# Optimization experiments

Measured on AMD Instinct MI355X. Metric: run time of the kernel, lower is better.

## Reference

```python
import jax, jax.numpy as jnp
import numpy as np

N = 120000   # hits
K = 512      # non-noise objects (ids 1..K; id 0 = noise)
D = 8        # cluster-space dim
C = 6        # pid classes
Q_MIN = 1.0
NOISE_THR = 0
PAYLOAD_W = 1.0
EPS = 1e-9


def setup_inputs() -> dict:
    key = jax.random.key(0)
    ks = jax.random.split(key, 9)
    beta = jax.random.uniform(ks[0], (N,), dtype=jnp.float32) * 0.95 + 0.01  # keep arctanh finite
    x = jax.random.normal(ks[1], (N, D), dtype=jnp.float32)
    object_id = jax.random.randint(ks[2], (N,), 0, K + 1).astype(jnp.int32)
    # guarantee every object id (and noise id 0) appears at least once
    object_id = object_id.at[: K + 1].set(jnp.arange(K + 1, dtype=jnp.int32))
    energy = jax.random.normal(ks[3], (N,), dtype=jnp.float32)
    energy_per_hit = jax.random.normal(ks[4], (N,), dtype=jnp.float32)
    momentum = jax.random.normal(ks[5], (N, 3), dtype=jnp.float32)
    momentum_per_hit = jax.random.normal(ks[6], (N, 3), dtype=jnp.float32)
    pid_logits = jax.random.normal(ks[7], (N, C), dtype=jnp.float32)
    pid_per_hit = jax.random.randint(ks[8], (N,), 0, C).astype(jnp.int32)
    return dict(beta=beta, x=x, object_id=object_id, energy=energy,
                energy_per_hit=energy_per_hit, momentum=momentum,
                momentum_per_hit=momentum_per_hit, pid_logits=pid_logits,
                pid_per_hit=pid_per_hit)


def _oc_core(beta, x, object_id):
    """condensation_loss_tiger with weights=1, max_n_rep=0 (no repulsive sampling)."""
    oids = jnp.arange(1, K + 1, dtype=object_id.dtype)
    att_mask = object_id[:, None] == oids[None, :]              # [N, K]
    q = jnp.arctanh(beta) ** 2 + Q_MIN                          # [N]
    alphas = jnp.argmax(q[:, None] * att_mask, axis=0)          # [K] condensation points
    x_k = x[alphas]                                             # [K, D]
    q_k = q[alphas]                                             # [K]
    # squared euclidean distance via gemm (avoids [N,K,D] intermediate)
    d2 = (jnp.sum(x * x, axis=1)[:, None] + jnp.sum(x_k * x_k, axis=1)[None, :]
          - 2.0 * (x @ x_k.T))
    d2 = jnp.maximum(d2, 0.0)                                   # [N, K]
    dist = jnp.sqrt(jnp.maximum(d2, 1e-12))
    qw = q[:, None] * q_k[None, :]                              # [N, K]
    # attractive: per-object normalized by hits in object, then mean over objects
    att_norm = jnp.sum(att_mask, axis=0).astype(x.dtype)        # [K]
    v_att = jnp.sum(jnp.where(att_mask, qw * d2, 0.0) / (att_norm + EPS)[None, :]) / K
    # repulsive: hinge (1 - dist), normalized by n_hits not in object
    rep_mask = (~att_mask) & (dist < 1.0)
    n_rep_k = jnp.sum(~att_mask, axis=0).astype(x.dtype)        # [K]
    n_rep = jnp.sum(rep_mask)
    v_rep = jnp.sum(jnp.where(rep_mask, qw * (1.0 - dist), 0.0) / (n_rep_k + EPS)[None, :]) / K
    l_coward = jnp.mean(1.0 - beta[alphas])
    noise_m = (object_id <= NOISE_THR).astype(beta.dtype)
    l_noise = jnp.sum(beta * noise_m) / jnp.sum(noise_m)
    return v_att, v_rep, l_coward, l_noise, n_rep


def reference(beta, x, object_id, energy, energy_per_hit, momentum,
              momentum_per_hit, pid_logits, pid_per_hit):
    v_att, v_rep, l_coward, l_noise, n_rep = _oc_core(beta, x, object_id)
    oc_total = v_att + v_rep + l_coward + l_noise
    # payload losses on non-noise hits (masked means == F.*_loss on gathered rows)
    m = (object_id > NOISE_THR).astype(beta.dtype)              # [N]
    nm = jnp.sum(m)
    e_loss = jnp.sum((energy - energy_per_hit) ** 2 * m) / nm
    p_loss = jnp.sum((momentum - momentum_per_hit) ** 2 * m[:, None]) / (nm * momentum.shape[1])
    logp = jax.nn.log_softmax(pid_logits, axis=-1)              # [N, C]
    nll = -jnp.take_along_axis(logp, pid_per_hit[:, None], axis=1)[:, 0]
    pid_loss = jnp.sum(nll * m) / nm
    total = oc_total + PAYLOAD_W * (e_loss + p_loss + pid_loss)
    return (v_att, v_rep, l_coward, l_noise, n_rep.astype(jnp.float32),
            oc_total, e_loss, p_loss, pid_loss, total)
```

## Files before the change

kernel.cpp:

```cpp
#include <hip/hip_runtime.h>
#include <math.h>

#define KOBJ 512
#define KTW 8
#define TK 32
#define NTILE (KOBJ / TK)
#define HB 8
#define HCH (256 * HB)
#define MPREP 128

typedef _Float16 half2_t __attribute__((ext_vector_type(2)));

#define AGS(p, v) __hip_atomic_store((p), (v), __ATOMIC_RELAXED, __HIP_MEMORY_SCOPE_AGENT)
#define AGL(p)    __hip_atomic_load((p), __ATOMIC_RELAXED, __HIP_MEMORY_SCOPE_AGENT)

__device__ __forceinline__ float wave_red_f(float v) {
  #pragma unroll
  for (int off = 32; off > 0; off >>= 1) v += __shfl_down(v, off, 64);
  return v;
}

__device__ __forceinline__ float q_of_beta(float b) {
  float a = 0.5f * __logf((1.f + b) / (1.f - b));
  return fmaf(a, a, 1.f);
}

__device__ __forceinline__ float dot8h(uint4 kx, const uint* y, float acc) {
#if __has_builtin(__builtin_amdgcn_fdot2)
  acc = __builtin_amdgcn_fdot2(__builtin_bit_cast(half2_t, y[0]),
                               __builtin_bit_cast(half2_t, kx.x), acc, false);
  acc = __builtin_amdgcn_fdot2(__builtin_bit_cast(half2_t, y[1]),
                               __builtin_bit_cast(half2_t, kx.y), acc, false);
  acc = __builtin_amdgcn_fdot2(__builtin_bit_cast(half2_t, y[2]),
                               __builtin_bit_cast(half2_t, kx.z), acc, false);
  acc = __builtin_amdgcn_fdot2(__builtin_bit_cast(half2_t, y[3]),
                               __builtin_bit_cast(half2_t, kx.w), acc, false);
#else
  const uint kk[4] = {kx.x, kx.y, kx.z, kx.w};
  #pragma unroll
  for (int c = 0; c < 4; c++) {
    half2_t a = __builtin_bit_cast(half2_t, y[c]);
    half2_t b = __builtin_bit_cast(half2_t, kk[c]);
    acc = fmaf((float)a.x, (float)b.x, acc);
    acc = fmaf((float)a.y, (float)b.y, acc);
  }
#endif
  return acc;
}

__global__ __launch_bounds__(256) void
k_prep(const float* __restrict__ beta, const int* __restrict__ oid,
       const float* __restrict__ energy, const float* __restrict__ eph,
       const float* __restrict__ mom, const float* __restrict__ mph,
       const float* __restrict__ logits, const int* __restrict__ pid,
       unsigned long long* __restrict__ amax_part,
       unsigned* __restrict__ cnt_part,
       float* __restrict__ scal_part,
       unsigned* __restrict__ done_cnt, int n) {
  __shared__ unsigned long long lmax[KOBJ];
  __shared__ unsigned lcnt[KOBJ];
  if (blockIdx.x == 0 && threadIdx.x == 0) *done_cnt = 0u;
  for (int t = threadIdx.x; t < KOBJ; t += 256) { lmax[t] = 0ull; lcnt[t] = 0u; }
  __syncthreads();

  float e_t = 0.f, p_t = 0.f, pid_t = 0.f, noise_t = 0.f, ncnt = 0.f, mcnt = 0.f;
  for (int i = blockIdx.x * 256 + threadIdx.x; i < n; i += MPREP * 256) {
    float b = beta[i];
    int o = oid[i];
    if (o > 0) {
      float q = q_of_beta(b);
      unsigned long long key = ((unsigned long long)__float_as_uint(q) << 32)
                             | (unsigned long long)(unsigned)(~(unsigned)i);
      atomicMax(&lmax[o - 1], key);
      atomicAdd(&lcnt[o - 1], 1u);
      mcnt += 1.f;
      float de = energy[i] - eph[i];
      e_t = fmaf(de, de, e_t);
      float p0 = mom[3*i+0] - mph[3*i+0];
      float p1 = mom[3*i+1] - mph[3*i+1];
      float p2 = mom[3*i+2] - mph[3*i+2];
      p_t = fmaf(p0, p0, p_t); p_t = fmaf(p1, p1, p_t); p_t = fmaf(p2, p2, p_t);
      const float* lg = logits + 6*i;
      float l0=lg[0], l1=lg[1], l2=lg[2], l3=lg[3], l4=lg[4], l5=lg[5];
      float mx = fmaxf(fmaxf(fmaxf(l0,l1),fmaxf(l2,l3)), fmaxf(l4,l5));
      float s = __expf(l0-mx)+__expf(l1-mx)+__expf(l2-mx)
              + __expf(l3-mx)+__expf(l4-mx)+__expf(l5-mx);
      int pc = pid[i];
      float lp = (pc==0)?l0:(pc==1)?l1:(pc==2)?l2:(pc==3)?l3:(pc==4)?l4:l5;
      pid_t += mx + __logf(s) - lp;
    } else {
      noise_t += b;
      ncnt += 1.f;
    }
  }
  __syncthreads();

  for (int t = threadIdx.x; t < KOBJ; t += 256) {
    amax_part[(size_t)blockIdx.x * KOBJ + t] = lmax[t];
    cnt_part[(size_t)blockIdx.x * KOBJ + t]  = lcnt[t];
  }

  float vals[6] = {e_t, p_t, pid_t, noise_t, ncnt, mcnt};
  #pragma unroll
  for (int j = 0; j < 6; j++) vals[j] = wave_red_f(vals[j]);
  __shared__ float sred[4][6];
  int w = threadIdx.x >> 6, l = threadIdx.x & 63;
  if (l == 0) {
    #pragma unroll
    for (int j = 0; j < 6; j++) sred[w][j] = vals[j];
  }
  __syncthreads();
  if (threadIdx.x == 0) {
    #pragma unroll
    for (int j = 0; j < 6; j++)
      scal_part[blockIdx.x * 8 + j] = sred[0][j]+sred[1][j]+sred[2][j]+sred[3][j];
  }
}

__global__ __launch_bounds__(256, 4) void
k_main(const float* __restrict__ x, const float* __restrict__ beta,
       const int* __restrict__ oid,
       const unsigned long long* __restrict__ amax_part,
       const unsigned* __restrict__ cnt_part,
       const float* __restrict__ scal_part,
       float* __restrict__ cow_part, float* __restrict__ pairs_part,
       unsigned* __restrict__ done_cnt, float* __restrict__ out, int n) {
  __shared__ __align__(16) uint skt[TK * KTW];
  __shared__ unsigned long long skey[8][32];
  __shared__ unsigned scnt_s[8][32];
  __shared__ float sredu[4][10];
  __shared__ unsigned slast;

  const int tid = threadIdx.x;
  const int w = tid >> 6, l = tid & 63;
  const int tile0 = blockIdx.y * TK;
  const int hbase = blockIdx.x * HCH;
  const int nblk = gridDim.x * gridDim.y;
  const int bid = blockIdx.y * gridDim.x + blockIdx.x;

  {
    int ko = tid & 31, seg = tid >> 5;
    unsigned long long key = 0ull;
    unsigned cnt = 0u;
    for (int m = seg; m < MPREP; m += 8) {
      unsigned long long km = amax_part[(size_t)m * KOBJ + tile0 + ko];
      key = (km > key) ? km : key;
      cnt += cnt_part[(size_t)m * KOBJ + tile0 + ko];
    }
    skey[seg][ko] = key;
    scnt_s[seg][ko] = cnt;
    __syncthreads();
    float cowv = 0.f;
    if (tid < 32) {
      #pragma unroll
      for (int c = 1; c < 8; c++) {
        unsigned long long kc = skey[c][tid];
        key = (kc > key) ? kc : key;
        cnt += scnt_s[c][tid];
      }
      unsigned idx = ~(unsigned)(key & 0xffffffffull);
      float q_k = __uint_as_float((unsigned)(key >> 32));
      const float4* xp4 = (const float4*)x;
      float4 xa = xp4[2 * (size_t)idx];
      float4 xb = xp4[2 * (size_t)idx + 1];
      float xv[8] = {xa.x, xa.y, xa.z, xa.w, xb.x, xb.y, xb.z, xb.w};
      float s2 = 0.f;
      #pragma unroll
      for (int c = 0; c < 8; c++) s2 = fmaf(xv[c], xv[c], s2);
      uint* kt = &skt[tid * KTW];
      #pragma unroll
      for (int c = 0; c < 4; c++) {
        half2_t hp = { (_Float16)xv[2*c], (_Float16)xv[2*c+1] };
        kt[c] = __builtin_bit_cast(uint, hp);
      }
      kt[4] = __float_as_uint(s2);
      kt[5] = __float_as_uint(q_k / ((float)(n - (int)cnt) + 1e-9f));
      kt[6] = __float_as_uint(q_k / ((float)cnt + 1e-9f));
      if (blockIdx.x == 0) cowv = 1.f - beta[idx];
    }
    if (tid < 64) {
      cowv = wave_red_f(cowv);
      if (tid == 0 && blockIdx.x == 0) AGS(&cow_part[blockIdx.y], cowv);
    }
    __syncthreads();
  }

  uint yh[HB][4];
  float thr[HB], bh2[HB], qi[HB];
  int own[HB];
  const float4* xp = (const float4*)x;
  #pragma unroll
  for (int h = 0; h < HB; h++) {
    int i = hbase + h * 256 + tid;
    if (i < n) {
      float4 xa = xp[2 * (size_t)i];
      float4 xb = xp[2 * (size_t)i + 1];
      float xi[8] = {xa.x, xa.y, xa.z, xa.w, xb.x, xb.y, xb.z, xb.w};
      float s = 0.f;
      #pragma unroll
      for (int c = 0; c < 8; c++) s = fmaf(xi[c], xi[c], s);
      bh2[h] = s;
      thr[h] = 1.f - s;
      #pragma unroll
      for (int c = 0; c < 4; c++) {
        half2_t hy = { (_Float16)(-2.f * xi[2*c]), (_Float16)(-2.f * xi[2*c+1]) };
        yh[h][c] = __builtin_bit_cast(uint, hy);
      }
      qi[h] = q_of_beta(beta[i]);
      own[h] = oid[i] - 1 - tile0;
    } else {
      #pragma unroll
      for (int c = 0; c < 4; c++) yh[h][c] = 0u;
      bh2[h] = 0.f;
      thr[h] = -1e30f;
      qi[h] = 0.f;
      own[h] = -1;
    }
  }

  float att = 0.f, rep = 0.f, nrep = 0.f;
  #pragma unroll 2
  for (int k2 = 0; k2 < TK; k2++) {
    const uint* kr = &skt[k2 * KTW];
    uint4 kx = *(const uint4*)kr;
    float s2 = __uint_as_float(kr[4]);
    float wr = __uint_as_float(kr[5]);
    #pragma unroll
    for (int h = 0; h < HB; h++) {
      float dp = dot8h(kx, yh[h], s2);
      if (dp < thr[h]) {
        float d2 = dp + bh2[h];
        float dist = sqrtf(fmaxf(d2, 1e-12f));
        rep = fmaf(qi[h] * (1.f - dist), wr, rep);
        nrep += 1.f;
      }
    }
  }

  #pragma unroll
  for (int h = 0; h < HB; h++) {
    int ko = own[h];
    if (ko >= 0 && ko < TK) {
      const uint* kr = &skt[ko * KTW];
      uint4 kx = *(const uint4*)kr;
      float s2 = __uint_as_float(kr[4]);
      float wr = __uint_as_float(kr[5]);
      float wa = __uint_as_float(kr[6]);
      float dp = dot8h(kx, yh[h], s2);
      float d2 = dp + bh2[h];
      att = fmaf(qi[h] * fmaxf(d2, 0.f), wa, att);
      if (dp < thr[h]) {
        float dist = sqrtf(fmaxf(d2, 1e-12f));
        rep = fmaf(-qi[h] * (1.f - dist), wr, rep);
        nrep -= 1.f;
      }
    }
  }

  att = wave_red_f(att);
  rep = wave_red_f(rep);
  nrep = wave_red_f(nrep);
  if (l == 0) { sredu[w][0] = att; sredu[w][1] = rep; sredu[w][2] = nrep; }
  __syncthreads();
  if (tid == 0) {
    AGS(&pairs_part[bid * 4 + 0], sredu[0][0]+sredu[1][0]+sredu[2][0]+sredu[3][0]);
    AGS(&pairs_part[bid * 4 + 1], sredu[0][1]+sredu[1][1]+sredu[2][1]+sredu[3][1]);
    AGS(&pairs_part[bid * 4 + 2], sredu[0][2]+sredu[1][2]+sredu[2][2]+sredu[3][2]);
    slast = __hip_atomic_fetch_add(done_cnt, 1u, __ATOMIC_ACQ_REL,
                                   __HIP_MEMORY_SCOPE_AGENT);
  }
  __syncthreads();

  if (slast == (unsigned)(nblk - 1)) {
    float v[10] = {0,0,0,0,0,0,0,0,0,0};
    for (int b2 = tid; b2 < nblk; b2 += 256) {
      v[0] += AGL(&pairs_part[b2 * 4 + 0]);
      v[1] += AGL(&pairs_part[b2 * 4 + 1]);
      v[2] += AGL(&pairs_part[b2 * 4 + 2]);
    }
    for (int m = tid; m < MPREP; m += 256) {
      #pragma unroll
      for (int j = 0; j < 6; j++) v[3 + j] += scal_part[m * 8 + j];
    }
    for (int g = tid; g < NTILE; g += 256) v[9] += AGL(&cow_part[g]);
    #pragma unroll
    for (int j = 0; j < 10; j++) v[j] = wave_red_f(v[j]);
    __syncthreads();
    if (l == 0) {
      #pragma unroll
      for (int j = 0; j < 10; j++) sredu[w][j] = v[j];
    }
    __syncthreads();
    if (tid == 0) {
      float t10[10];
      #pragma unroll
      for (int j = 0; j < 10; j++)
        t10[j] = sredu[0][j]+sredu[1][j]+sredu[2][j]+sredu[3][j];
      float v_att  = t10[0] / (float)KOBJ;
      float v_rep  = t10[1] / (float)KOBJ;
      float n_rep  = t10[2];
      float l_cow  = t10[9] / (float)KOBJ;
      float l_noise = t10[6] / t10[7];
      float oc = v_att + v_rep + l_cow + l_noise;
      float nm = t10[8];
      float e_loss  = t10[3] / nm;
      float p_loss  = t10[4] / (nm * 3.f);
      float pid_loss = t10[5] / nm;
      out[0] = v_att;
      out[1] = v_rep;
      out[2] = l_cow;
      out[3] = l_noise;
      out[4] = n_rep;
      out[5] = oc;
      out[6] = e_loss;
      out[7] = p_loss;
      out[8] = pid_loss;
      out[9] = oc + e_loss + p_loss + pid_loss;
    }
  }
}

extern "C" void kernel_launch(void* const* d_in, const int* in_sizes, int n_in,
                              void* d_out, int out_size, void* d_ws, size_t ws_size,
                              hipStream_t stream) {
  const float* beta   = (const float*)d_in[0];
  const float* x      = (const float*)d_in[1];
  const int*   oid    = (const int*)d_in[2];
  const float* energy = (const float*)d_in[3];
  const float* eph    = (const float*)d_in[4];
  const float* mom    = (const float*)d_in[5];
  const float* mph    = (const float*)d_in[6];
  const float* logits = (const float*)d_in[7];
  const int*   pid    = (const int*)d_in[8];
  float* outp = (float*)d_out;
  const int n = in_sizes[0];
  const int nhb = (n + HCH - 1) / HCH;
  const int nblk_tot = nhb * NTILE;

  char* base = (char*)d_ws;
  size_t off = 0;
  float* cow_part   = (float*)(base + off); off += (size_t)NTILE * 4;
  float* pairs_part = (float*)(base + off); off += (size_t)nblk_tot * 4 * 4;
  float* scal_part  = (float*)(base + off); off += (size_t)MPREP * 8 * 4;
  unsigned* done_cnt = (unsigned*)(base + off); off += 256;
  off = (off + 255) & ~(size_t)255;
  unsigned long long* amax_part = (unsigned long long*)(base + off); off += (size_t)MPREP * KOBJ * 8;
  unsigned* cnt_part = (unsigned*)(base + off);                      off += (size_t)MPREP * KOBJ * 4;

  k_prep<<<MPREP, 256, 0, stream>>>(beta, oid, energy, eph, mom, mph, logits, pid,
                                    amax_part, cnt_part, scal_part, done_cnt, n);
  k_main<<<dim3(nhb, NTILE), 256, 0, stream>>>(x, beta, oid, amax_part, cnt_part,
                                               scal_part, cow_part, pairs_part,
                                               done_cnt, outp, n);
}
```

Baseline: 121.2 us.

## Precompute packed half-precision hit records in prep kernel; halve hits per block

```diff
diff --git a/kernel.cpp b/kernel.cpp
--- a/kernel.cpp
+++ b/kernel.cpp
@@ -5,7 +5,7 @@
 #define KTW 8
 #define TK 32
 #define NTILE (KOBJ / TK)
-#define HB 8
+#define HB 4
 #define HCH (256 * HB)
 #define MPREP 128
 
@@ -49,13 +49,15 @@
 }
 
 __global__ __launch_bounds__(256) void
-k_prep(const float* __restrict__ beta, const int* __restrict__ oid,
+k_prep(const float* __restrict__ beta, const float* __restrict__ x,
+       const int* __restrict__ oid,
        const float* __restrict__ energy, const float* __restrict__ eph,
        const float* __restrict__ mom, const float* __restrict__ mph,
        const float* __restrict__ logits, const int* __restrict__ pid,
        unsigned long long* __restrict__ amax_part,
        unsigned* __restrict__ cnt_part,
        float* __restrict__ scal_part,
+       uint4* __restrict__ hry, uint4* __restrict__ hrm,
        unsigned* __restrict__ done_cnt, int n) {
   __shared__ unsigned long long lmax[KOBJ];
   __shared__ unsigned lcnt[KOBJ];
@@ -63,12 +65,34 @@
   for (int t = threadIdx.x; t < KOBJ; t += 256) { lmax[t] = 0ull; lcnt[t] = 0u; }
   __syncthreads();
 
+  const float4* xp = (const float4*)x;
   float e_t = 0.f, p_t = 0.f, pid_t = 0.f, noise_t = 0.f, ncnt = 0.f, mcnt = 0.f;
   for (int i = blockIdx.x * 256 + threadIdx.x; i < n; i += MPREP * 256) {
     float b = beta[i];
     int o = oid[i];
+    float q = q_of_beta(b);
+    float4 xa = xp[2 * (size_t)i];
+    float4 xb = xp[2 * (size_t)i + 1];
+    float xi[8] = {xa.x, xa.y, xa.z, xa.w, xb.x, xb.y, xb.z, xb.w};
+    float s = 0.f;
+    #pragma unroll
+    for (int c = 0; c < 8; c++) s = fmaf(xi[c], xi[c], s);
+    uint4 r0;
+    {
+      half2_t h0 = { (_Float16)(-2.f * xi[0]), (_Float16)(-2.f * xi[1]) };
+      half2_t h1 = { (_Float16)(-2.f * xi[2]), (_Float16)(-2.f * xi[3]) };
+      half2_t h2 = { (_Float16)(-2.f * xi[4]), (_Float16)(-2.f * xi[5]) };
+      half2_t h3 = { (_Float16)(-2.f * xi[6]), (_Float16)(-2.f * xi[7]) };
+      r0.x = __builtin_bit_cast(uint, h0);
+      r0.y = __builtin_bit_cast(uint, h1);
+      r0.z = __builtin_bit_cast(uint, h2);
+      r0.w = __builtin_bit_cast(uint, h3);
+    }
+    uint4 r1 = { __float_as_uint(s), __float_as_uint(q), (uint)o, 0u };
+    hry[i] = r0;
+    hrm[i] = r1;
+
     if (o > 0) {
-      float q = q_of_beta(b);
       unsigned long long key = ((unsigned long long)__float_as_uint(q) << 32)
                              | (unsigned long long)(unsigned)(~(unsigned)i);
       atomicMax(&lmax[o - 1], key);
@@ -83,11 +107,11 @@
       const float* lg = logits + 6*i;
       float l0=lg[0], l1=lg[1], l2=lg[2], l3=lg[3], l4=lg[4], l5=lg[5];
       float mx = fmaxf(fmaxf(fmaxf(l0,l1),fmaxf(l2,l3)), fmaxf(l4,l5));
-      float s = __expf(l0-mx)+__expf(l1-mx)+__expf(l2-mx)
-              + __expf(l3-mx)+__expf(l4-mx)+__expf(l5-mx);
+      float sm = __expf(l0-mx)+__expf(l1-mx)+__expf(l2-mx)
+               + __expf(l3-mx)+__expf(l4-mx)+__expf(l5-mx);
       int pc = pid[i];
       float lp = (pc==0)?l0:(pc==1)?l1:(pc==2)?l2:(pc==3)?l3:(pc==4)?l4:l5;
-      pid_t += mx + __logf(s) - lp;
+      pid_t += mx + __logf(sm) - lp;
     } else {
       noise_t += b;
       ncnt += 1.f;
@@ -117,15 +141,15 @@
   }
 }
 
-__global__ __launch_bounds__(256, 4) void
+__global__ __launch_bounds__(256, 8) void
 k_main(const float* __restrict__ x, const float* __restrict__ beta,
-       const int* __restrict__ oid,
+       const uint4* __restrict__ hry, const uint4* __restrict__ hrm,
        const unsigned long long* __restrict__ amax_part,
        const unsigned* __restrict__ cnt_part,
        const float* __restrict__ scal_part,
        float* __restrict__ cow_part, float* __restrict__ pairs_part,
        unsigned* __restrict__ done_cnt, float* __restrict__ out, int n) {
-  __shared__ __align__(16) uint skt[TK * KTW];
+  __shared__ __align__(16) uint skt[(TK + 1) * KTW];
   __shared__ unsigned long long skey[8][32];
   __shared__ unsigned scnt_s[8][32];
   __shared__ float sredu[4][10];
@@ -176,8 +200,10 @@
       kt[4] = __float_as_uint(s2);
       kt[5] = __float_as_uint(q_k / ((float)(n - (int)cnt) + 1e-9f));
       kt[6] = __float_as_uint(q_k / ((float)cnt + 1e-9f));
+      kt[7] = 0u;
       if (blockIdx.x == 0) cowv = 1.f - beta[idx];
     }
+    if (tid < 8) skt[TK * KTW + tid] = 0u;
     if (tid < 64) {
       cowv = wave_red_f(cowv);
       if (tid == 0 && blockIdx.x == 0) AGS(&cow_part[blockIdx.y], cowv);
@@ -188,26 +214,18 @@
   uint yh[HB][4];
   float thr[HB], bh2[HB], qi[HB];
   int own[HB];
-  const float4* xp = (const float4*)x;
   #pragma unroll
   for (int h = 0; h < HB; h++) {
     int i = hbase + h * 256 + tid;
     if (i < n) {
-      float4 xa = xp[2 * (size_t)i];
-      float4 xb = xp[2 * (size_t)i + 1];
-      float xi[8] = {xa.x, xa.y, xa.z, xa.w, xb.x, xb.y, xb.z, xb.w};
-      float s = 0.f;
-      #pragma unroll
-      for (int c = 0; c < 8; c++) s = fmaf(xi[c], xi[c], s);
+      uint4 ra = hry[i];
+      uint4 rb = hrm[i];
+      yh[h][0] = ra.x; yh[h][1] = ra.y; yh[h][2] = ra.z; yh[h][3] = ra.w;
+      float s = __uint_as_float(rb.x);
       bh2[h] = s;
       thr[h] = 1.f - s;
-      #pragma unroll
-      for (int c = 0; c < 4; c++) {
-        half2_t hy = { (_Float16)(-2.f * xi[2*c]), (_Float16)(-2.f * xi[2*c+1]) };
-        yh[h][c] = __builtin_bit_cast(uint, hy);
-      }
-      qi[h] = q_of_beta(beta[i]);
-      own[h] = oid[i] - 1 - tile0;
+      qi[h] = __uint_as_float(rb.y);
+      own[h] = (int)rb.z - 1 - tile0;
     } else {
       #pragma unroll
       for (int c = 0; c < 4; c++) yh[h][c] = 0u;
@@ -219,15 +237,17 @@
   }
 
   float att = 0.f, rep = 0.f, nrep = 0.f;
+  const uint4* skt4 = (const uint4*)skt;
+  uint4 kxa = skt4[0], kxb = skt4[1];
   #pragma unroll 2
   for (int k2 = 0; k2 < TK; k2++) {
-    const uint* kr = &skt[k2 * KTW];
-    uint4 kx = *(const uint4*)kr;
-    float s2 = __uint_as_float(kr[4]);
-    float wr = __uint_as_float(kr[5]);
+    uint4 nxa = skt4[2 * k2 + 2];
+    uint4 nxb = skt4[2 * k2 + 3];
+    float s2 = __uint_as_float(kxb.x);
+    float wr = __uint_as_float(kxb.y);
     #pragma unroll
     for (int h = 0; h < HB; h++) {
-      float dp = dot8h(kx, yh[h], s2);
+      float dp = dot8h(kxa, yh[h], s2);
       if (dp < thr[h]) {
         float d2 = dp + bh2[h];
         float dist = sqrtf(fmaxf(d2, 1e-12f));
@@ -235,18 +255,19 @@
         nrep += 1.f;
       }
     }
+    kxa = nxa; kxb = nxb;
   }
 
   #pragma unroll
   for (int h = 0; h < HB; h++) {
     int ko = own[h];
     if (ko >= 0 && ko < TK) {
-      const uint* kr = &skt[ko * KTW];
-      uint4 kx = *(const uint4*)kr;
-      float s2 = __uint_as_float(kr[4]);
-      float wr = __uint_as_float(kr[5]);
-      float wa = __uint_as_float(kr[6]);
-      float dp = dot8h(kx, yh[h], s2);
+      uint4 ka = skt4[2 * ko];
+      uint4 kb = skt4[2 * ko + 1];
+      float s2 = __uint_as_float(kb.x);
+      float wr = __uint_as_float(kb.y);
+      float wa = __uint_as_float(kb.z);
+      float dp = dot8h(ka, yh[h], s2);
       float d2 = dp + bh2[h];
       att = fmaf(qi[h] * fmaxf(d2, 0.f), wa, att);
       if (dp < thr[h]) {
@@ -346,10 +367,14 @@
   off = (off + 255) & ~(size_t)255;
   unsigned long long* amax_part = (unsigned long long*)(base + off); off += (size_t)MPREP * KOBJ * 8;
   unsigned* cnt_part = (unsigned*)(base + off);                      off += (size_t)MPREP * KOBJ * 4;
-
-  k_prep<<<MPREP, 256, 0, stream>>>(beta, oid, energy, eph, mom, mph, logits, pid,
-                                    amax_part, cnt_part, scal_part, done_cnt, n);
-  k_main<<<dim3(nhb, NTILE), 256, 0, stream>>>(x, beta, oid, amax_part, cnt_part,
+  off = (off + 255) & ~(size_t)255;
+  uint4* hry = (uint4*)(base + off); off += (size_t)(nhb * HCH) * 16;
+  uint4* hrm = (uint4*)(base + off); off += (size_t)(nhb * HCH) * 16;
+
+  k_prep<<<MPREP, 256, 0, stream>>>(beta, x, oid, energy, eph, mom, mph, logits, pid,
+                                    amax_part, cnt_part, scal_part, hry, hrm,
+                                    done_cnt, n);
+  k_main<<<dim3(nhb, NTILE), 256, 0, stream>>>(x, beta, hry, hrm, amax_part, cnt_part,
                                                scal_part, cow_part, pairs_part,
                                                done_cnt, outp, n);
 }
```

After: 133.6 us. 10.3% more time.
